# Performance work log

Measured on AMD Instinct MI355X. Metric: run time of the kernel, lower is better.

The kernel has to match this reference:

```python
import jax, jax.numpy as jnp
import numpy as np

N, E, IN, HID, OUT = 50000, 800000, 256, 256, 64
HEADS, DH = 4, 64  # GAT: hidden//4 per head, concat=False -> mean over heads
EPS = 1e-5


def _gcn(x, W, b, src, dst):
    # PyG GCNConv: h = xW; add self-loops; sym-normalized scatter-add; + bias
    n = x.shape[0]
    h = x @ W
    deg = jnp.zeros((n,), x.dtype).at[dst].add(1.0) + 1.0  # +1 for self-loop
    dinv = jax.lax.rsqrt(deg)
    norm = dinv[src] * dinv[dst]                      # [E]
    out = jax.ops.segment_sum(h[src] * norm[:, None], dst, num_segments=n)
    out = out + h * (dinv * dinv)[:, None]            # self-loop term
    return out + b


def _gat(x, W, a_s, a_d, b, src, dst):
    # PyG GATConv(heads=HEADS, concat=False): per-edge attention softmax over
    # incoming edges (incl. self-loop), LeakyReLU(0.2) logits, mean over heads.
    n = x.shape[0]
    h = (x @ W).reshape(n, HEADS, DH)
    al_s = jnp.einsum('nhd,hd->nh', h, a_s)           # [N,H]
    al_d = jnp.einsum('nhd,hd->nh', h, a_d)
    e = jax.nn.leaky_relu(al_s[src] + al_d[dst], 0.2)  # [E,H]
    e_self = jax.nn.leaky_relu(al_s + al_d, 0.2)       # [N,H]
    m = jnp.maximum(jax.ops.segment_max(e, dst, num_segments=n), e_self)
    ee = jnp.exp(e - m[dst])
    es = jnp.exp(e_self - m)
    denom = jax.ops.segment_sum(ee, dst, num_segments=n) + es        # [N,H]
    numer = jax.ops.segment_sum(ee[:, :, None] * h[src], dst, num_segments=n) + es[:, :, None] * h
    return (numer / denom[:, :, None]).mean(axis=1) + b


def _bn(x, g, b):
    # BatchNorm1d over node dim, batch statistics (training-mode math)
    mu = x.mean(axis=0)
    var = x.var(axis=0)
    return g * (x - mu) * jax.lax.rsqrt(var + EPS) + b


def setup_inputs() -> dict:
    key = jax.random.key(0)
    ks = jax.random.split(key, 12)
    s = lambda d: 1.0 / np.sqrt(d)
    inp = {
        'x': jax.random.normal(ks[0], (N, IN), jnp.float32),
        'edge_index': jax.random.randint(ks[1], (2, E), 0, N, jnp.int64),
        'W1': jax.random.normal(ks[2], (IN, HID), jnp.float32) * s(IN),
        'b1': jnp.zeros((HID,), jnp.float32),
        'g1': jnp.ones((HID,), jnp.float32),
        'be1': jnp.zeros((HID,), jnp.float32),
        'Wg': jax.random.normal(ks[3], (HID, HEADS * DH), jnp.float32) * s(HID),
        'a_src': jax.random.normal(ks[4], (HEADS, DH), jnp.float32) * s(DH),
        'a_dst': jax.random.normal(ks[5], (HEADS, DH), jnp.float32) * s(DH),
        'bg': jnp.zeros((DH,), jnp.float32),
        'g2': jnp.ones((DH,), jnp.float32),
        'be2': jnp.zeros((DH,), jnp.float32),
        'W3': jax.random.normal(ks[6], (64, 16), jnp.float32) * s(64),
        'b3': jnp.zeros((16,), jnp.float32),
        'g3': jnp.ones((16,), jnp.float32),
        'be3': jnp.zeros((16,), jnp.float32),
        'W4': jax.random.normal(ks[7], (16, OUT), jnp.float32) * s(16),
        'b4': jnp.zeros((OUT,), jnp.float32),
        'r1W': jax.random.normal(ks[8], (IN, HID), jnp.float32) * s(IN),
        'r1b': jnp.zeros((HID,), jnp.float32),
        'r2W': jax.random.normal(ks[9], (HID, 64), jnp.float32) * s(HID),
        'r2b': jnp.zeros((64,), jnp.float32),
        'r3W': jax.random.normal(ks[10], (64, 16), jnp.float32) * s(64),
        'r3b': jnp.zeros((16,), jnp.float32),
        'pW': jax.random.normal(ks[11], (OUT, OUT), jnp.float32) * s(OUT),
        'pb': jnp.zeros((OUT,), jnp.float32),
    }
    return inp


def reference(x, edge_index, W1, b1, g1, be1, Wg, a_src, a_dst, bg, g2, be2,
              W3, b3, g3, be3, W4, b4, r1W, r1b, r2W, r2b, r3W, r3b, pW, pb):
    src, dst = edge_index[0], edge_index[1]
    slope = 0.01  # F.leaky_relu default; dropout is identity at inference
    x0 = x
    h = _gcn(x0, W1, b1, src, dst)
    h = jax.nn.leaky_relu(_bn(h, g1, be1), slope)
    h = h + (x0 @ r1W + r1b)
    x2 = h
    h = _gat(x2, Wg, a_src, a_dst, bg, src, dst)
    h = jax.nn.leaky_relu(_bn(h, g2, be2), slope)
    h = h + (x2 @ r2W + r2b)
    x3 = h
    h = _gcn(x3, W3, b3, src, dst)
    h = jax.nn.leaky_relu(_bn(h, g3, be3), slope)
    h = h + (x3 @ r3W + r3b)
    h = _gcn(h, W4, b4, src, dst)
    return h @ pW + pb
```

## Files before the change

kernel.cpp:

```cpp
#include <hip/hip_runtime.h>

typedef unsigned short u16;
typedef unsigned int   u32;

__device__ __forceinline__ float b2f(u16 h){ return __uint_as_float(((u32)h)<<16); }
__device__ __forceinline__ u16 f2b(float f){
  u32 u = __float_as_uint(f);
  u32 r = (u + 0x7fffu + ((u>>16)&1u)) >> 16;
  return (u16)r;
}
__device__ __forceinline__ float leaky(float x, float s){ return x >= 0.f ? x : s*x; }

typedef __bf16 bf16x8 __attribute__((ext_vector_type(8)));
typedef float  f32x4  __attribute__((ext_vector_type(4)));

__device__ __forceinline__ float ldval(const u16* p){ return b2f(*p); }
__device__ __forceinline__ float ldval(const float* p){ return *p; }

__device__ __forceinline__ void load8(const u16* p, u16* h){ *(uint4*)h = *(const uint4*)p; }
__device__ __forceinline__ void load8(const float* p, u16* h){
  float4 a = *(const float4*)p; float4 b = *(const float4*)(p+4);
  h[0]=f2b(a.x); h[1]=f2b(a.y); h[2]=f2b(a.z); h[3]=f2b(a.w);
  h[4]=f2b(b.x); h[5]=f2b(b.y); h[6]=f2b(b.z); h[7]=f2b(b.w);
}

__global__ void k_detect(const u32* __restrict__ w, int E, u32* __restrict__ flag){
  u32 acc = 0;
  for (int i = blockIdx.x*256 + threadIdx.x; i < E; i += 256*gridDim.x)
    acc |= w[2*i + 1];
  __shared__ u32 s[256];
  s[threadIdx.x] = acc; __syncthreads();
  for (int o=128;o>0;o>>=1){ if (threadIdx.x<o) s[threadIdx.x] |= s[threadIdx.x+o]; __syncthreads(); }
  if (threadIdx.x==0 && s[0]) atomicOr(flag, 1u);
}

__device__ __forceinline__ void edge_sd(const int* __restrict__ ei, int E, int e, u32 is32,
                                        int& s, int& d){
  if (is32){ s = ei[e];   d = ei[E + e]; }
  else     { s = ei[2*e]; d = ei[2*E + 2*e]; }
}

__global__ void k_hist(const int* __restrict__ ei, int E, int nN,
                       const u32* __restrict__ flag, int* __restrict__ cnt){
  int e = blockIdx.x*256 + threadIdx.x;
  if (e < E){
    int s,d; edge_sd(ei, E, e, *flag, s, d);
    if ((u32)s < (u32)nN && (u32)d < (u32)nN) atomicAdd(&cnt[d], 1);
  }
}

__global__ void k_scan_a(const int* __restrict__ cnt, int n, int* __restrict__ bsum){
  __shared__ int s[256];
  int base = blockIdx.x*1024, t = threadIdx.x, sum = 0;
  for (int j=0;j<4;j++){ int i = base + t*4 + j; if (i<n) sum += cnt[i]; }
  s[t] = sum; __syncthreads();
  for (int off=128; off>0; off>>=1){ if (t<off) s[t]+=s[t+off]; __syncthreads(); }
  if (t==0) bsum[blockIdx.x] = s[0];
}

__global__ void k_scan_b(int* bsum, int nb){
  if (threadIdx.x==0 && blockIdx.x==0){
    int acc = 0;
    for (int i=0;i<nb;i++){ int v = bsum[i]; bsum[i] = acc; acc += v; }
  }
}

__global__ void k_scan_c(const int* __restrict__ cnt, const int* __restrict__ bsum,
                         int n, int* __restrict__ offs){
  __shared__ int s[256];
  int base = blockIdx.x*1024, t = threadIdx.x;
  int v[4]; int sum=0;
  for (int j=0;j<4;j++){ int i=base+t*4+j; v[j] = (i<n)?cnt[i]:0; sum += v[j]; }
  s[t]=sum; __syncthreads();
  for (int off=1; off<256; off<<=1){
    int add = (t>=off)? s[t-off] : 0;
    __syncthreads();
    s[t] += add;
    __syncthreads();
  }
  int excl = (t ? s[t-1] : 0) + bsum[blockIdx.x];
  for (int j=0;j<4;j++){
    int i = base+t*4+j;
    if (i<n){ offs[i] = excl; excl += v[j]; if (i==n-1) offs[n] = excl; }
  }
}

__global__ void k_dinv2(const int* __restrict__ offs, int n, float* __restrict__ dinv){
  int i = blockIdx.x*256+threadIdx.x;
  if (i<n) dinv[i] = rsqrtf((float)(offs[i+1]-offs[i]) + 1.0f);
}

__global__ void k_scatter(const int* __restrict__ ei, int E, int nN,
                          const u32* __restrict__ flag, const int* __restrict__ offs,
                          int* __restrict__ cursor, int* __restrict__ csr){
  int e = blockIdx.x*256+threadIdx.x;
  if (e<E){
    int s,d; edge_sd(ei, E, e, *flag, s, d);
    if ((u32)s < (u32)nN && (u32)d < (u32)nN){
      int pos = offs[d] + atomicAdd(&cursor[d], 1);
      csr[pos] = s;
    }
  }
}

__global__ void k_transpose(const float* __restrict__ in, u16* __restrict__ out, int K, int M){
  int i = blockIdx.x*256 + threadIdx.x;
  if (i < K*M){ int k = i / M, m = i % M; out[m*K + k] = f2b(in[i]); }
}

__global__ void k_asdt(const float* __restrict__ a_s, const float* __restrict__ a_d,
                       float* __restrict__ asi, float* __restrict__ adi){
  int i = threadIdx.x;
  int h = i>>6, c = i&63;
  asi[c*4+h] = a_s[i];
  adi[c*4+h] = a_d[i];
}

template<typename AT>
__global__ __launch_bounds__(256) void k_gemm64(
  const AT* __restrict__ A0, const AT* __restrict__ A1,
  const AT* __restrict__ A2, const AT* __restrict__ A3,
  int rsA, const u16* __restrict__ Bt, const float* __restrict__ bias,
  u16* __restrict__ out, int nRows)
{
  alignas(16) __shared__ u16 Al[64*264];
  const int t = threadIdx.x;
  const int r0 = blockIdx.x*64;
  for (int it=0; it<8; ++it){
    int c = t + it*256;
    int row = c>>5, seg = c&31;
    int gr = r0+row;
    u16 hv[8] = {0,0,0,0,0,0,0,0};
    if (gr < nRows){
      const AT* p = (seg<8)?A0 : (seg<16)?A1 : (seg<24)?A2 : A3;
      load8(p + (size_t)gr*rsA + (seg&7)*8, hv);
    }
    *(uint4*)&Al[row*264 + seg*8] = *(uint4*)hv;
  }
  const int lane=t&63, wid=t>>6, quad=lane>>4, l15=lane&15;
  __syncthreads();
  const int col = wid*16 + l15;
  const u16* Bp = Bt + (size_t)col*256 + quad*8;
  bf16x8 b[8];
  #pragma unroll
  for (int ks=0;ks<8;++ks) b[ks] = *(const bf16x8*)(Bp + ks*32);
  f32x4 acc[4] = {{0.f,0.f,0.f,0.f},{0.f,0.f,0.f,0.f},{0.f,0.f,0.f,0.f},{0.f,0.f,0.f,0.f}};
  #pragma unroll
  for (int rt=0; rt<4; ++rt){
    const int abase = (rt*16 + l15)*264 + quad*8;
    #pragma unroll
    for (int ks=0;ks<8;++ks){
      bf16x8 av = *(const bf16x8*)&Al[abase + ks*32];
      acc[rt] = __builtin_amdgcn_mfma_f32_16x16x32_bf16(av, b[ks], acc[rt], 0,0,0);
    }
  }
  __syncthreads();
  float bv = bias ? bias[col] : 0.f;
  #pragma unroll
  for (int rt=0; rt<4; ++rt){
    #pragma unroll
    for (int reg=0;reg<4;++reg)
      Al[(rt*16 + quad*4 + reg)*264 + col] = f2b(acc[rt][reg]+bv);
  }
  __syncthreads();
  #pragma unroll
  for (int it=0; it<2; ++it){
    int idx = it*256 + t;
    int row = idx>>3, cu = idx&7;
    if (r0+row < nRows)
      *(uint4*)(out + (size_t)(r0+row)*64 + cu*8) = *(const uint4*)&Al[row*264 + cu*8];
  }
}

template<typename AT, bool PERM>
__global__ __launch_bounds__(256) void k_gemm256(
  const AT* __restrict__ A0, const AT* __restrict__ A1,
  const AT* __restrict__ A2, const AT* __restrict__ A3,
  int rsA, const u16* __restrict__ Bt, const float* __restrict__ bias,
  u16* __restrict__ out, int nRows)
{
  alignas(16) __shared__ u16 Al[64*264];
  const int t = threadIdx.x;
  const int r0 = blockIdx.x*64;
  for (int it=0; it<8; ++it){
    int c = t + it*256;
    int row = c>>5, seg = c&31;
    int gr = r0+row;
    u16 hv[8] = {0,0,0,0,0,0,0,0};
    if (gr < nRows){
      const AT* p = (seg<8)?A0 : (seg<16)?A1 : (seg<24)?A2 : A3;
      load8(p + (size_t)gr*rsA + (seg&7)*8, hv);
    }
    *(uint4*)&Al[row*264 + seg*8] = *(uint4*)hv;
  }
  const int lane=t&63, wid=t>>6, quad=lane>>4, l15=lane&15;
  __syncthreads();
  f32x4 acc[4][4];
  #pragma unroll
  for (int ct=0; ct<4; ++ct)
    #pragma unroll
    for (int rt=0; rt<4; ++rt) acc[ct][rt] = {0.f,0.f,0.f,0.f};
  #pragma unroll
  for (int ct=0; ct<4; ++ct){
    const u16* Bp = Bt + (size_t)(wid*64 + ct*16 + l15)*256 + quad*8;
    bf16x8 b[8];
    #pragma unroll
    for (int ks=0;ks<8;++ks) b[ks] = *(const bf16x8*)(Bp + ks*32);
    #pragma unroll
    for (int rt=0; rt<4; ++rt){
      const int abase = (rt*16 + l15)*264 + quad*8;
      #pragma unroll
      for (int ks=0;ks<8;++ks){
        bf16x8 av = *(const bf16x8*)&Al[abase + ks*32];
        acc[ct][rt] = __builtin_amdgcn_mfma_f32_16x16x32_bf16(av, b[ks], acc[ct][rt], 0,0,0);
      }
    }
  }
  __syncthreads();
  #pragma unroll
  for (int ct=0; ct<4; ++ct){
    int col = wid*64 + ct*16 + l15;
    float bv = bias ? bias[col] : 0.f;
    int oc = PERM ? ((col&63)*4 + (col>>6)) : col;
    #pragma unroll
    for (int rt=0; rt<4; ++rt){
      #pragma unroll
      for (int reg=0;reg<4;++reg)
        Al[(rt*16 + quad*4 + reg)*264 + oc] = f2b(acc[ct][rt][reg]+bv);
    }
  }
  __syncthreads();
  #pragma unroll
  for (int it=0; it<8; ++it){
    int idx = it*256 + t;
    int row = idx>>5, cu = idx&31;
    if (r0+row < nRows)
      *(uint4*)(out + (size_t)(r0+row)*256 + cu*8) = *(const uint4*)&Al[row*264 + cu*8];
  }
}

__global__ void k_gather64(const u16* __restrict__ h, const int* __restrict__ offs,
                           const int* __restrict__ csr, const float* __restrict__ dinv,
                           const float* __restrict__ bias, int n, u16* __restrict__ out){
  int nd = blockIdx.x*4 + (threadIdx.x>>6);
  if (nd>=n) return;
  int lane = threadIdx.x&63;
  float dn = dinv[nd];
  float acc = dn*b2f(h[(size_t)nd*64+lane]);
  int e = offs[nd], end = offs[nd+1];
  for (; e+4<=end; e+=4){
    int s0=csr[e], s1=csr[e+1], s2=csr[e+2], s3=csr[e+3];
    float w0=dinv[s0], w1=dinv[s1], w2=dinv[s2], w3=dinv[s3];
    float p0=b2f(h[(size_t)s0*64+lane]);
    float p1=b2f(h[(size_t)s1*64+lane]);
    float p2=b2f(h[(size_t)s2*64+lane]);
    float p3=b2f(h[(size_t)s3*64+lane]);
    acc += w0*p0 + w1*p1 + w2*p2 + w3*p3;
  }
  for (; e<end; ++e){
    int s=csr[e];
    acc += dinv[s]*b2f(h[(size_t)s*64+lane]);
  }
  out[(size_t)nd*64+lane] = f2b(dn*acc + bias[lane]);
}

__global__ void k_gather256(const u16* __restrict__ h, const int* __restrict__ offs,
                            const int* __restrict__ csr, const float* __restrict__ dinv,
                            const float* __restrict__ bias, int n, u16* __restrict__ out){
  int nd = blockIdx.x*4 + (threadIdx.x>>6);
  if (nd>=n) return;
  int lane = threadIdx.x&63;
  const uint2* H = (const uint2*)h;
  float dn = dinv[nd];
  uint2 pv = H[(size_t)nd*64 + lane];
  float a0=dn*b2f(pv.x&0xffff), a1=dn*b2f(pv.x>>16);
  float a2=dn*b2f(pv.y&0xffff), a3=dn*b2f(pv.y>>16);
  int e=offs[nd], end=offs[nd+1];
  for (; e+2<=end; e+=2){
    int s0=csr[e], s1=csr[e+1];
    float w0=dinv[s0], w1=dinv[s1];
    uint2 q0=H[(size_t)s0*64+lane], q1=H[(size_t)s1*64+lane];
    a0 += w0*b2f(q0.x&0xffff) + w1*b2f(q1.x&0xffff);
    a1 += w0*b2f(q0.x>>16)    + w1*b2f(q1.x>>16);
    a2 += w0*b2f(q0.y&0xffff) + w1*b2f(q1.y&0xffff);
    a3 += w0*b2f(q0.y>>16)    + w1*b2f(q1.y>>16);
  }
  for (; e<end; ++e){
    int s=csr[e]; float w=dinv[s];
    uint2 q=H[(size_t)s*64+lane];
    a0 += w*b2f(q.x&0xffff); a1 += w*b2f(q.x>>16);
    a2 += w*b2f(q.y&0xffff); a3 += w*b2f(q.y>>16);
  }
  float4 bv = *(const float4*)(bias + lane*4);
  uint2 o;
  o.x = (u32)f2b(a0*dn + bv.x) | ((u32)f2b(a1*dn + bv.y)<<16);
  o.y = (u32)f2b(a2*dn + bv.z) | ((u32)f2b(a3*dn + bv.w)<<16);
  ((uint2*)out)[(size_t)nd*64 + lane] = o;
}

template<typename T, int C>
__global__ __launch_bounds__(256) void k_stats_part(const T* __restrict__ x, int n,
                                                    float* __restrict__ part){
  constexpr int VE = 16/sizeof(T);
  constexpr int G  = C/VE;
  constexpr int R  = 256/G;
  int t = threadIdx.x;
  int g = t % G, sub = t / G;
  int rpb = (n + gridDim.x - 1) / gridDim.x;
  int base = blockIdx.x * rpb;
  int lim  = min(base + rpb, n);
  float s[VE], s2[VE];
  #pragma unroll
  for (int j=0;j<VE;j++){ s[j]=0.f; s2[j]=0.f; }
  #pragma unroll 4
  for (int r = base + sub; r < lim; r += R){
    const T* p = x + (size_t)r*C + g*VE;
    if constexpr (sizeof(T)==2){
      uint4 v = *(const uint4*)p;
      u32 wq[4] = {v.x, v.y, v.z, v.w};
      #pragma unroll
      for (int q=0;q<4;q++){
        float lo = __uint_as_float(wq[q]<<16);
        float hi = __uint_as_float(wq[q]&0xffff0000u);
        s[2*q]  += lo; s2[2*q]  += lo*lo;
        s[2*q+1]+= hi; s2[2*q+1]+= hi*hi;
      }
    } else {
      float4 v = *(const float4*)p;
      float a[4] = {v.x, v.y, v.z, v.w};
      #pragma unroll
      for (int q=0;q<4;q++){ s[q]+=a[q]; s2[q]+=a[q]*a[q]; }
    }
  }
  __shared__ float red[VE][256];
  #pragma unroll
  for (int j=0;j<VE;j++) red[j][t] = s[j];
  __syncthreads();
  for (int off=R/2; off>0; off>>=1){
    if (sub < off){
      #pragma unroll
      for (int j=0;j<VE;j++) red[j][t] += red[j][t + off*G];
    }
    __syncthreads();
  }
  if (t < G){
    #pragma unroll
    for (int j=0;j<VE;j++) part[blockIdx.x*2*C + t*VE + j] = red[j][t];
  }
  __syncthreads();
  #pragma unroll
  for (int j=0;j<VE;j++) red[j][t] = s2[j];
  __syncthreads();
  for (int off=R/2; off>0; off>>=1){
    if (sub < off){
      #pragma unroll
      for (int j=0;j<VE;j++) red[j][t] += red[j][t + off*G];
    }
    __syncthreads();
  }
  if (t < G){
    #pragma unroll
    for (int j=0;j<VE;j++) part[blockIdx.x*2*C + C + t*VE + j] = red[j][t];
  }
}

template<int C>
__global__ __launch_bounds__(256) void k_bnfin3(const float* __restrict__ part, int B,
                         const float* __restrict__ g, const float* __restrict__ be,
                         float n, float* __restrict__ bnp){
  constexpr int CPB = (C < 32) ? C : 32;
  constexpr int TPC = 256 / CPB;
  int t = threadIdx.x;
  int lc = t % CPB, sub = t / CPB;
  int c = blockIdx.x*CPB + lc;
  float s=0.f, s2=0.f;
  for (int b = sub; b < B; b += TPC){
    s  += part[(size_t)b*2*C + c];
    s2 += part[(size_t)b*2*C + C + c];
  }
  __shared__ float ls[256], lq[256];
  ls[t]=s; lq[t]=s2; __syncthreads();
  for (int off=TPC/2; off>0; off>>=1){
    if (sub < off){ ls[t]+=ls[t+off*CPB]; lq[t]+=lq[t+off*CPB]; }
    __syncthreads();
  }
  if (sub==0){
    float mu = ls[t]/n;
    float var = fmaxf(lq[t]/n - mu*mu, 0.f);
    float sc = g[c] * rsqrtf(var + 1e-5f);
    bnp[c] = sc;
    bnp[C+c] = be[c] - mu*sc;
  }
}

__global__ void k_ew_b16b16(const u16* __restrict__ agg, const u16* __restrict__ res,
                            const float* __restrict__ bnp, int C, int total, u16* __restrict__ out){
  int i = blockIdx.x*256+threadIdx.x;
  if (i < total){
    int c = i & (C-1);
    float v = b2f(agg[i])*bnp[c] + bnp[C+c];
    out[i] = f2b(leaky(v, 0.01f) + b2f(res[i]));
  }
}

__global__ void k_ew_f32f32(const float* __restrict__ agg, const float* __restrict__ res,
                            const float* __restrict__ bnp, int C, int total, float* __restrict__ out){
  int i = blockIdx.x*256+threadIdx.x;
  if (i < total){
    int c = i & (C-1);
    float v = agg[i]*bnp[c] + bnp[C+c];
    out[i] = leaky(v, 0.01f) + res[i];
  }
}

__global__ void k_dot64(const u16* __restrict__ h2t, const float* __restrict__ asg,
                        const float* __restrict__ adg, int head, int n,
                        float* __restrict__ als, float* __restrict__ ald){
  int nd = blockIdx.x*4 + (threadIdx.x>>6);
  if (nd>=n) return;
  int lane = threadIdx.x&63;
  float p = b2f(h2t[(size_t)nd*64+lane]);
  float ss = p*asg[lane];
  float sd = p*adg[lane];
  for (int m=1;m<64;m<<=1){ ss += __shfl_xor(ss,m,64); sd += __shfl_xor(sd,m,64); }
  if (lane==0){ als[nd*4+head]=ss; ald[nd*4+head]=sd; }
}

__global__ void k_gat_head(const u16* __restrict__ h2t, const int* __restrict__ offs,
                           const int* __restrict__ csr, const float* __restrict__ als,
                           const float* __restrict__ ald, const float* __restrict__ bg,
                           int head, int n, u16* __restrict__ O2){
  int nd = blockIdx.x*4 + (threadIdx.x>>6);
  if (nd>=n) return;
  int lane = threadIdx.x&63;
  float aldn = ald[nd*4+head];
  float m = leaky(als[nd*4+head] + aldn, 0.2f);
  float denom = 1.f;
  float acc = b2f(h2t[(size_t)nd*64+lane]);
  int e = offs[nd], end = offs[nd+1];
  for (; e+4<=end; e+=4){
    int s0=csr[e], s1=csr[e+1], s2=csr[e+2], s3=csr[e+3];
    float l0=als[s0*4+head], l1=als[s1*4+head], l2=als[s2*4+head], l3=als[s3*4+head];
    float p0=b2f(h2t[(size_t)s0*64+lane]);
    float p1=b2f(h2t[(size_t)s1*64+lane]);
    float p2=b2f(h2t[(size_t)s2*64+lane]);
    float p3=b2f(h2t[(size_t)s3*64+lane]);
    float g0=leaky(l0+aldn,0.2f), g1=leaky(l1+aldn,0.2f);
    float g2=leaky(l2+aldn,0.2f), g3=leaky(l3+aldn,0.2f);
    float mc = fmaxf(fmaxf(g0,g1), fmaxf(g2,g3));
    float mn = fmaxf(m, mc);
    float sc = __expf(m - mn);
    float w0 = __expf(g0-mn), w1 = __expf(g1-mn), w2 = __expf(g2-mn), w3 = __expf(g3-mn);
    denom = denom*sc + (w0+w1+w2+w3);
    acc   = acc*sc   + (w0*p0 + w1*p1 + w2*p2 + w3*p3);
    m = mn;
  }
  for (; e<end; ++e){
    int s = csr[e];
    float g = leaky(als[s*4+head]+aldn, 0.2f);
    float p = b2f(h2t[(size_t)s*64+lane]);
    float mn = fmaxf(m, g);
    float sc = __expf(m - mn);
    float w = __expf(g - mn);
    denom = denom*sc + w;
    acc   = acc*sc   + w*p;
    m = mn;
  }
  float v = 0.25f * acc / fmaxf(denom, 1e-20f);
  size_t oi = (size_t)nd*64+lane;
  if (head==0) O2[oi] = f2b(v + bg[lane]);
  else         O2[oi] = f2b(b2f(O2[oi]) + v);
}

__global__ void k_dot_all(const u16* __restrict__ h2i, const float* __restrict__ asi,
                          const float* __restrict__ adi, int n,
                          float* __restrict__ als, float* __restrict__ ald){
  int nd = blockIdx.x*4 + (threadIdx.x>>6);
  if (nd>=n) return;
  int lane = threadIdx.x&63;
  uint2 pv = ((const uint2*)h2i)[(size_t)nd*64+lane];
  float p0=b2f(pv.x&0xffff), p1=b2f(pv.x>>16), p2=b2f(pv.y&0xffff), p3=b2f(pv.y>>16);
  float4 as4 = *(const float4*)(asi + lane*4);
  float4 ad4 = *(const float4*)(adi + lane*4);
  float s0=p0*as4.x, s1=p1*as4.y, s2=p2*as4.z, s3=p3*as4.w;
  float d0=p0*ad4.x, d1=p1*ad4.y, d2=p2*ad4.z, d3=p3*ad4.w;
  for (int m=1;m<64;m<<=1){
    s0+=__shfl_xor(s0,m,64); s1+=__shfl_xor(s1,m,64);
    s2+=__shfl_xor(s2,m,64); s3+=__shfl_xor(s3,m,64);
    d0+=__shfl_xor(d0,m,64); d1+=__shfl_xor(d1,m,64);
    d2+=__shfl_xor(d2,m,64); d3+=__shfl_xor(d3,m,64);
  }
  if (lane==0){
    float4 sv = {s0,s1,s2,s3}; float4 dv = {d0,d1,d2,d3};
    ((float4*)als)[nd] = sv;
    ((float4*)ald)[nd] = dv;
  }
}

__global__ void k_gat_all(const u16* __restrict__ h2i, const int* __restrict__ offs,
                          const int* __restrict__ csr, const float* __restrict__ als,
                          const float* __restrict__ ald, const float* __restrict__ bg,
                          int n, u16* __restrict__ O2){
  alignas(16) __shared__ float shm[4][80];
  int wv = threadIdx.x>>6;
  int nd = blockIdx.x*4 + wv;
  if (nd>=n) return;
  int lane = threadIdx.x&63;
  int eg = lane>>2, hh = lane&3;
  float4 alv = ((const float4*)als)[nd];
  float4 adv = ((const float4*)ald)[nd];
  float adh = (hh&2) ? ((hh&1)?adv.w:adv.z) : ((hh&1)?adv.y:adv.x);
  float alh = (hh&2) ? ((hh&1)?alv.w:alv.z) : ((hh&1)?alv.y:alv.x);
  float gsh = leaky(alh+adh, 0.2f);
  int beg=offs[nd], end=offs[nd+1];
  float m = gsh;
  for (int e=beg+eg; e<end; e+=16){
    int s = csr[e];
    m = fmaxf(m, leaky(als[s*4+hh]+adh, 0.2f));
  }
  #pragma unroll
  for (int off=4; off<64; off<<=1) m = fmaxf(m, __shfl_xor(m, off, 64));
  float wsh = __expf(gsh - m);
  if (eg==0) shm[wv][4+hh] = wsh;
  float4 ws4 = *(const float4*)&shm[wv][4];
  uint2 pv = ((const uint2*)h2i)[(size_t)nd*64+lane];
  float a0 = ws4.x*__uint_as_float(pv.x<<16);
  float a1 = ws4.y*__uint_as_float(pv.x&0xffff0000u);
  float a2 = ws4.z*__uint_as_float(pv.y<<16);
  float a3 = ws4.w*__uint_as_float(pv.y&0xffff0000u);
  float dpart = 0.f;
  const uint2* H = (const uint2*)h2i;
  for (int e0=beg; e0<end; e0+=16){
    int e = e0+eg;
    int sA = 0; float wE = 0.f;
    if (e<end){
      sA = csr[e];
      wE = __expf(leaky(als[sA*4+hh]+adh, 0.2f) - m);
    }
    dpart += wE;
    shm[wv][8+lane] = wE;
    int cnt = min(16, end-e0);
    int k=0;
    for (; k+4<=cnt; k+=4){
      int sa=__shfl(sA,(k  )*4,64), sb=__shfl(sA,(k+1)*4,64);
      int sc=__shfl(sA,(k+2)*4,64), sd=__shfl(sA,(k+3)*4,64);
      float4 wa=*(const float4*)&shm[wv][8+(k  )*4];
      float4 wb=*(const float4*)&shm[wv][8+(k+1)*4];
      float4 wc=*(const float4*)&shm[wv][8+(k+2)*4];
      float4 wd=*(const float4*)&shm[wv][8+(k+3)*4];
      uint2 qa=H[(size_t)sa*64+lane], qb=H[(size_t)sb*64+lane];
      uint2 qc=H[(size_t)sc*64+lane], qd=H[(size_t)sd*64+lane];
      a0 += wa.x*__uint_as_float(qa.x<<16) + wb.x*__uint_as_float(qb.x<<16)
          + wc.x*__uint_as_float(qc.x<<16) + wd.x*__uint_as_float(qd.x<<16);
      a1 += wa.y*__uint_as_float(qa.x&0xffff0000u) + wb.y*__uint_as_float(qb.x&0xffff0000u)
          + wc.y*__uint_as_float(qc.x&0xffff0000u) + wd.y*__uint_as_float(qd.x&0xffff0000u);
      a2 += wa.z*__uint_as_float(qa.y<<16) + wb.z*__uint_as_float(qb.y<<16)
          + wc.z*__uint_as_float(qc.y<<16) + wd.z*__uint_as_float(qd.y<<16);
      a3 += wa.w*__uint_as_float(qa.y&0xffff0000u) + wb.w*__uint_as_float(qb.y&0xffff0000u)
          + wc.w*__uint_as_float(qc.y&0xffff0000u) + wd.w*__uint_as_float(qd.y&0xffff0000u);
    }
    for (; k<cnt; ++k){
      int s = __shfl(sA, k*4, 64);
      float4 w4 = *(const float4*)&shm[wv][8+k*4];
      uint2 q = H[(size_t)s*64+lane];
      a0 += w4.x*__uint_as_float(q.x<<16);
      a1 += w4.y*__uint_as_float(q.x&0xffff0000u);
      a2 += w4.z*__uint_as_float(q.y<<16);
      a3 += w4.w*__uint_as_float(q.y&0xffff0000u);
    }
  }
  #pragma unroll
  for (int off=4; off<64; off<<=1) dpart += __shfl_xor(dpart, off, 64);
  float dh = dpart + wsh;
  if (eg==0) shm[wv][hh] = dh;
  float4 d4 = *(const float4*)&shm[wv][0];
  float v = 0.25f*(a0/d4.x + a1/d4.y + a2/d4.z + a3/d4.w);
  O2[(size_t)nd*64+lane] = f2b(v + bg[lane]);
}

__global__ void k_gcn_agg16(const float* __restrict__ h, const int* __restrict__ offs,
                            const int* __restrict__ csr, const float* __restrict__ dinv,
                            const float* __restrict__ bias, float* __restrict__ out, int n){
  int t = threadIdx.x;
  int nd = blockIdx.x*16 + (t>>4);
  if (nd>=n) return;
  int c = t&15;
  float dn = dinv[nd];
  float acc = dn*h[(size_t)nd*16+c];
  int e=offs[nd], end=offs[nd+1];
  for (; e+4<=end; e+=4){
    int s0=csr[e], s1=csr[e+1], s2=csr[e+2], s3=csr[e+3];
    float w0=dinv[s0], w1=dinv[s1], w2=dinv[s2], w3=dinv[s3];
    float p0=h[(size_t)s0*16+c], p1=h[(size_t)s1*16+c];
    float p2=h[(size_t)s2*16+c], p3=h[(size_t)s3*16+c];
    acc += w0*p0 + w1*p1 + w2*p2 + w3*p3;
  }
  for (; e<end; ++e){
    int s = csr[e];
    acc += dinv[s]*h[(size_t)s*16+c];
  }
  out[(size_t)nd*16+c] = dn*acc + bias[c];
}

__global__ void k_gcn_agg64f(const float* __restrict__ h, const int* __restrict__ offs,
                             const int* __restrict__ csr, const float* __restrict__ dinv,
                             const float* __restrict__ bias, float* __restrict__ out, int n){
  int nd = blockIdx.x*4 + (threadIdx.x>>6);
  if (nd>=n) return;
  int lane = threadIdx.x&63;
  float dn = dinv[nd];
  float acc = dn*h[(size_t)nd*64+lane];
  int e=offs[nd], end=offs[nd+1];
  for (; e+4<=end; e+=4){
    int s0=csr[e], s1=csr[e+1], s2=csr[e+2], s3=csr[e+3];
    float w0=dinv[s0], w1=dinv[s1], w2=dinv[s2], w3=dinv[s3];
    float p0=h[(size_t)s0*64+lane], p1=h[(size_t)s1*64+lane];
    float p2=h[(size_t)s2*64+lane], p3=h[(size_t)s3*64+lane];
    acc += w0*p0 + w1*p1 + w2*p2 + w3*p3;
  }
  for (; e<end; ++e){
    int s=csr[e];
    acc += dinv[s]*h[(size_t)s*64+lane];
  }
  out[(size_t)nd*64+lane] = dn*acc + bias[lane];
}

__global__ void k_gemm64_16x2(const u16* __restrict__ x, const float* __restrict__ W1_,
                              const float* __restrict__ W2_, const float* __restrict__ b2_,
                              int n, float* __restrict__ o1, float* __restrict__ o2){
  __shared__ float w1[64*16], w2[64*16];
  int t = threadIdx.x;
  for (int i=t; i<1024; i+=256){ w1[i]=W1_[i]; w2[i]=W2_[i]; }
  __syncthreads();
  int nd = blockIdx.x*8 + (t>>5);
  if (nd>=n) return;
  int j = t & 31;
  const u16* xr = x + (size_t)nd*64;
  if (j<16){
    float s=0.f;
    #pragma unroll 8
    for (int k=0;k<64;k++) s += b2f(xr[k])*w1[k*16+j];
    o1[(size_t)nd*16+j]=s;
  } else {
    int jj=j-16;
    float s = b2_[jj];
    #pragma unroll 8
    for (int k=0;k<64;k++) s += b2f(xr[k])*w2[k*16+jj];
    o2[(size_t)nd*16+jj]=s;
  }
}

__global__ void k_gemm16_64(const float* __restrict__ x, const float* __restrict__ W,
                            int n, float* __restrict__ o){
  __shared__ float w[16*64];
  int t = threadIdx.x;
  for (int i=t;i<1024;i+=256) w[i]=W[i];
  __syncthreads();
  int nd = blockIdx.x*4 + (t>>6);
  if (nd>=n) return;
  int j = t&63;
  const float* xr = x + (size_t)nd*16;
  float s=0.f;
  #pragma unroll
  for (int k=0;k<16;k++) s += xr[k]*w[k*64+j];
  o[(size_t)nd*64+j]=s;
}

__global__ void k_final(const float* __restrict__ x, const float* __restrict__ W,
                        const float* __restrict__ b, int n, float* __restrict__ out){
  __shared__ float w[64*64];
  int t=threadIdx.x;
  for (int i=t;i<4096;i+=256) w[i]=W[i];
  __syncthreads();
  int nd = blockIdx.x*4 + (t>>6);
  if (nd>=n) return;
  int j=t&63;
  const float* xr = x + (size_t)nd*64;
  float s=b[j];
  #pragma unroll 8
  for (int k=0;k<64;k++) s += xr[k]*w[k*64+j];
  out[(size_t)nd*64+j]=s;
}

extern "C" void kernel_launch(void* const* d_in, const int* in_sizes, int n_in,
                              void* d_out, int out_size, void* d_ws, size_t ws_size,
                              hipStream_t stream) {
  const float* x   = (const float*)d_in[0];
  const int*   ei  = (const int*)d_in[1];
  const float* W1  = (const float*)d_in[2];
  const float* b1  = (const float*)d_in[3];
  const float* g1  = (const float*)d_in[4];
  const float* be1 = (const float*)d_in[5];
  const float* Wg  = (const float*)d_in[6];
  const float* a_s = (const float*)d_in[7];
  const float* a_d = (const float*)d_in[8];
  const float* bg  = (const float*)d_in[9];
  const float* g2  = (const float*)d_in[10];
  const float* be2 = (const float*)d_in[11];
  const float* W3  = (const float*)d_in[12];
  const float* b3  = (const float*)d_in[13];
  const float* g3  = (const float*)d_in[14];
  const float* be3 = (const float*)d_in[15];
  const float* W4  = (const float*)d_in[16];
  const float* b4  = (const float*)d_in[17];
  const float* r1W = (const float*)d_in[18];
  const float* r1b = (const float*)d_in[19];
  const float* r2W = (const float*)d_in[20];
  const float* r2b = (const float*)d_in[21];
  const float* r3W = (const float*)d_in[22];
  const float* r3b = (const float*)d_in[23];
  const float* pW  = (const float*)d_in[24];
  const float* pb  = (const float*)d_in[25];

  const int N = in_sizes[0] / 256;
  const int E = in_sizes[1] / 2;

  char* w = (char*)d_ws;
  auto alloc = [&](size_t b)->void*{ void* p=(void*)w; w += (b+255)&~(size_t)255; return p; };
  u32*   flag   = (u32*)  alloc(4);
  float* part   = (float*)alloc(256*512*4);
  float* bnp1   = (float*)alloc(512*4);
  float* bnp2   = (float*)alloc(128*4);
  float* bnp3   = (float*)alloc(32*4);
  int*   bsum   = (int*)  alloc(256*4);
  int*   cur    = (int*)  alloc((size_t)N*4);
  int*   offs   = (int*)  alloc((size_t)(N+1)*4);
  float* dinv   = (float*)alloc((size_t)N*4);
  int*   csr    = (int*)  alloc((size_t)E*4);
  float* als    = (float*)alloc((size_t)N*16);
  float* ald    = (float*)alloc((size_t)N*16);
  float* asi    = (float*)alloc(256*4);
  float* adi    = (float*)alloc(256*4);
  u16*   W1t    = (u16*)  alloc(65536*2);
  u16*   r1Wt   = (u16*)  alloc(65536*2);
  u16*   Wgt    = (u16*)  alloc(65536*2);
  u16*   r2Wt   = (u16*)  alloc(16384*2);

  auto cdiv = [](int a, int b){ return (a+b-1)/b; };
  const int nb1024 = cdiv(N, 1024);
  const int statsGrid = 256;
  const int gemmGrid = cdiv(N,64);
  const int nodeGrid = cdiv(N,4);

  hipMemsetAsync(flag,   0, 4, stream);
  hipMemsetAsync(cur,    0, (size_t)N*4, stream);

  k_detect<<<64,256,0,stream>>>((const u32*)ei, E, flag);

  k_transpose<<<cdiv(65536,256),256,0,stream>>>(W1,  W1t,  256,256);
  k_transpose<<<cdiv(65536,256),256,0,stream>>>(r1W, r1Wt, 256,256);
  k_transpose<<<cdiv(65536,256),256,0,stream>>>(Wg,  Wgt,  256,256);
  k_transpose<<<cdiv(16384,256),256,0,stream>>>(r2W, r2Wt, 256,64);
  k_asdt<<<1,256,0,stream>>>(a_s, a_d, asi, adi);

  k_hist  <<<cdiv(E,256),256,0,stream>>>(ei, E, N, flag, cur);
  k_scan_a<<<nb1024,256,0,stream>>>(cur, N, bsum);
  k_scan_b<<<1,64,0,stream>>>(bsum, nb1024);
  k_scan_c<<<nb1024,256,0,stream>>>(cur, bsum, N, offs);
  k_dinv2 <<<cdiv(N,256),256,0,stream>>>(offs, N, dinv);
  hipMemsetAsync(cur, 0, (size_t)N*4, stream);
  k_scatter<<<cdiv(E,256),256,0,stream>>>(ei, E, N, flag, offs, cur, csr);

  size_t miscUsed = (size_t)(w - (char*)d_ws);
  size_t bigNeed  = miscUsed + 2*((size_t)N*512) + 1024;

  if (ws_size >= bigNeed){
    u16* RA = (u16*)alloc((size_t)N*512);
    u16* RB = (u16*)alloc((size_t)N*512);
    u16* tAe = (u16*)d_in[1];
    u16* r2d = (u16*)d_out;

    float* h3   = (float*)RA;
    float* r3   = (float*)(RA + (size_t)N*32);
    float* agg3 = (float*)(RA + (size_t)N*64);
    float* x4   = (float*)(RA + (size_t)N*96);
    float* h4   = (float*)RB;
    float* agg4 = (float*)d_out;

    k_gemm256<float,false><<<gemmGrid,256,0,stream>>>(x, x+64, x+128, x+192, 256,
                                                      W1t, nullptr, RA, N);
    k_gather256<<<nodeGrid,256,0,stream>>>(RA, offs, csr, dinv, b1, N, RB);
    k_stats_part<u16,256><<<statsGrid,256,0,stream>>>(RB, N, part);
    k_bnfin3<256><<<8,256,0,stream>>>(part, statsGrid, g1, be1, (float)N, bnp1);
    k_gemm256<float,false><<<gemmGrid,256,0,stream>>>(x, x+64, x+128, x+192, 256,
                                                      r1Wt, r1b, RA, N);
    k_ew_b16b16<<<cdiv(N*256,256),256,0,stream>>>(RB, RA, bnp1, 256, N*256, RB);

    k_gemm256<u16,true><<<gemmGrid,256,0,stream>>>(RB, RB+64, RB+128, RB+192, 256,
                                                   Wgt, nullptr, RA, N);
    k_gemm64<u16><<<gemmGrid,256,0,stream>>>(RB, RB+64, RB+128, RB+192, 256,
                                             r2Wt, r2b, r2d, N);
    k_dot_all<<<nodeGrid,256,0,stream>>>(RA, asi, adi, N, als, ald);
    k_gat_all<<<nodeGrid,256,0,stream>>>(RA, offs, csr, als, ald, bg, N, tAe);
    k_stats_part<u16,64><<<statsGrid,256,0,stream>>>(tAe, N, part);
    k_bnfin3<64><<<2,256,0,stream>>>(part, statsGrid, g2, be2, (float)N, bnp2);
    k_ew_b16b16<<<cdiv(N*64,256),256,0,stream>>>(tAe, r2d, bnp2, 64, N*64, tAe);

    k_gemm64_16x2<<<cdiv(N,8),256,0,stream>>>(tAe, W3, r3W, r3b, N, h3, r3);
    k_gcn_agg16<<<cdiv(N,16),256,0,stream>>>(h3, offs, csr, dinv, b3, agg3, N);
    k_stats_part<float,16><<<statsGrid,256,0,stream>>>(agg3, N, part);
    k_bnfin3<16><<<1,256,0,stream>>>(part, statsGrid, g3, be3, (float)N, bnp3);
    k_ew_f32f32<<<cdiv(N*16,256),256,0,stream>>>(agg3, r3, bnp3, 16, N*16, x4);

    k_gemm16_64<<<nodeGrid,256,0,stream>>>(x4, W4, N, h4);
    k_gcn_agg64f<<<nodeGrid,256,0,stream>>>(h4, offs, csr, dinv, b4, agg4, N);
    k_final<<<nodeGrid,256,0,stream>>>(agg4, pW, pb, N, (float*)d_out);
  } else {
    u16* X0 = (u16*)alloc((size_t)N*64*2);
    u16* X1 = (u16*)alloc((size_t)N*64*2);
    u16* tA = (u16*)alloc((size_t)N*64*2);
    u16* tB = (u16*)alloc((size_t)N*64*2);
    u16* X2 = (u16*)d_in[1];
    u16* X3 = (u16*)d_out;
    const u16* XP[4] = {X0, X1, X2, X3};

    float* h3   = (float*)X1;
    float* r3   = (float*)(X1 + (size_t)N*32);
    float* agg3 = (float*)tA;
    float* x4   = (float*)(tA + (size_t)N*32);
    float* h4   = (float*)X0;
    float* agg4 = (float*)tA;

    for (int tau=0; tau<4; ++tau){
      u16* Xt = (u16*)XP[tau];
      k_gemm64<float><<<gemmGrid,256,0,stream>>>(x, x+64, x+128, x+192, 256,
                                                 W1t + (size_t)tau*64*256, nullptr, tA, N);
      k_gather64<<<nodeGrid,256,0,stream>>>(tA, offs, csr, dinv, b1 + tau*64, N, tB);
      k_stats_part<u16,64><<<statsGrid,256,0,stream>>>(tB, N, part);
      k_bnfin3<64><<<2,256,0,stream>>>(part, statsGrid, g1 + tau*64, be1 + tau*64, (float)N, bnp1 + tau*128);
      k_gemm64<float><<<gemmGrid,256,0,stream>>>(x, x+64, x+128, x+192, 256,
                                                 r1Wt + (size_t)tau*64*256, r1b + tau*64, tA, N);
      k_ew_b16b16<<<cdiv(N*64,256),256,0,stream>>>(tB, tA, bnp1 + tau*128, 64, N*64, Xt);
    }

    for (int head=0; head<4; ++head){
      k_gemm64<u16><<<gemmGrid,256,0,stream>>>(XP[0], XP[1], XP[2], XP[3], 64,
                                               Wgt + (size_t)head*64*256, nullptr, tA, N);
      k_dot64<<<nodeGrid,256,0,stream>>>(tA, a_s + head*64, a_d + head*64, head, N, als, ald);
      k_gat_head<<<nodeGrid,256,0,stream>>>(tA, offs, csr, als, ald, bg, head, N, tB);
    }
    k_gemm64<u16><<<gemmGrid,256,0,stream>>>(XP[0], XP[1], XP[2], XP[3], 64,
                                             r2Wt, r2b, tA, N);
    k_stats_part<u16,64><<<statsGrid,256,0,stream>>>(tB, N, part);
    k_bnfin3<64><<<2,256,0,stream>>>(part, statsGrid, g2, be2, (float)N, bnp2);
    k_ew_b16b16<<<cdiv(N*64,256),256,0,stream>>>(tB, tA, bnp2, 64, N*64, X0);

    k_gemm64_16x2<<<cdiv(N,8),256,0,stream>>>(X0, W3, r3W, r3b, N, h3, r3);
    k_gcn_agg16<<<cdiv(N,16),256,0,stream>>>(h3, offs, csr, dinv, b3, agg3, N);
    k_stats_part<float,16><<<statsGrid,256,0,stream>>>(agg3, N, part);
    k_bnfin3<16><<<1,256,0,stream>>>(part, statsGrid, g3, be3, (float)N, bnp3);
    k_ew_f32f32<<<cdiv(N*16,256),256,0,stream>>>(agg3, r3, bnp3, 16, N*16, x4);

    k_gemm16_64<<<nodeGrid,256,0,stream>>>(x4, W4, N, h4);
    k_gcn_agg64f<<<nodeGrid,256,0,stream>>>(h4, offs, csr, dinv, b4, agg4, N);
    k_final<<<nodeGrid,256,0,stream>>>(agg4, pW, pb, N, (float*)d_out);
  }
}
```

Baseline: 725.0 us.

## Split graph aggregation kernels across channel groups and parallel edge slices

Three CSR aggregation kernels (GCN layer-1 gather, the GAT attention aggregation, and the final 64-wide GCN aggregation) are replaced with variants that split each node's channels into groups handled by separate blocks. Each wave also processes four edges at once in 16-lane slices, followed by shuffle reductions. The aim is more memory-level parallelism and a larger grid for the irregular neighbour gathers, with nontemporal loads on the CSR indices. The cost is redundant reads of CSR, dinv and attention logits across channel groups, extra shuffles, and in GAT a repeated max pass per group.

```diff
diff --git a/kernel.cpp b/kernel.cpp
--- a/kernel.cpp
+++ b/kernel.cpp
@@ -262,6 +262,47 @@
     acc += dinv[s]*b2f(h[(size_t)s*64+lane]);
   }
   out[(size_t)nd*64+lane] = f2b(dn*acc + bias[lane]);
+}
+
+__global__ __launch_bounds__(256) void k_gather256x(const u16* __restrict__ h, const int* __restrict__ offs,
+                              const int* __restrict__ csr, const float* __restrict__ dinv,
+                              const float* __restrict__ bias, int n, u16* __restrict__ out){
+  int bid = blockIdx.x;
+  int cg = bid & 7, tile = bid >> 3;
+  int nd = tile*4 + (threadIdx.x>>6);
+  if (nd>=n) return;
+  int lane = threadIdx.x & 63;
+  int es = lane >> 4, li = lane & 15;
+  const u32* H = (const u32*)h;
+  const int coff = cg*16 + li;
+  float dn = dinv[nd];
+  float a0 = 0.f, a1 = 0.f;
+  if (es == 0){
+    u32 pv = H[(size_t)nd*128 + coff];
+    a0 = dn*b2f(pv&0xffff); a1 = dn*b2f(pv>>16);
+  }
+  int e = offs[nd] + es, end = offs[nd+1];
+  for (; e + 4 < end; e += 8){
+    int s0 = __builtin_nontemporal_load(&csr[e]);
+    int s1 = __builtin_nontemporal_load(&csr[e+4]);
+    float w0 = dinv[s0], w1 = dinv[s1];
+    u32 q0 = H[(size_t)s0*128 + coff], q1 = H[(size_t)s1*128 + coff];
+    a0 += w0*b2f(q0&0xffff) + w1*b2f(q1&0xffff);
+    a1 += w0*b2f(q0>>16)    + w1*b2f(q1>>16);
+  }
+  if (e < end){
+    int s = __builtin_nontemporal_load(&csr[e]);
+    float w = dinv[s];
+    u32 q = H[(size_t)s*128 + coff];
+    a0 += w*b2f(q&0xffff); a1 += w*b2f(q>>16);
+  }
+  a0 += __shfl_xor(a0,16,64); a0 += __shfl_xor(a0,32,64);
+  a1 += __shfl_xor(a1,16,64); a1 += __shfl_xor(a1,32,64);
+  if (es == 0){
+    int c = cg*32 + li*2;
+    u32 o = (u32)f2b(a0*dn + bias[c]) | ((u32)f2b(a1*dn + bias[c+1])<<16);
+    ((u32*)out)[(size_t)nd*128 + coff] = o;
+  }
 }
 
 __global__ void k_gather256(const u16* __restrict__ h, const int* __restrict__ offs,
@@ -497,6 +538,77 @@
   }
 }
 
+__global__ __launch_bounds__(256) void k_gat_allx(const u16* __restrict__ h2i, const int* __restrict__ offs,
+                           const int* __restrict__ csr, const float* __restrict__ als,
+                           const float* __restrict__ ald, const float* __restrict__ bg,
+                           int n, u16* __restrict__ O2){
+  int bid = blockIdx.x;
+  int cg = bid & 7, tile = bid >> 3;
+  int nd = tile*4 + (threadIdx.x>>6);
+  if (nd>=n) return;
+  int lane = threadIdx.x & 63;
+  int es = lane >> 4, li = lane & 15;
+  int hh = lane & 3;
+  int h0 = (li & 1) << 1, h1 = h0 + 1;
+  float4 alv = ((const float4*)als)[nd];
+  float4 adv = ((const float4*)ald)[nd];
+  float adh = (hh&2) ? ((hh&1)?adv.w:adv.z) : ((hh&1)?adv.y:adv.x);
+  float alh = (hh&2) ? ((hh&1)?alv.w:alv.z) : ((hh&1)?alv.y:alv.x);
+  float gsh = leaky(alh+adh, 0.2f);
+  int beg = offs[nd], end = offs[nd+1];
+  float m = gsh;
+  for (int e = beg+es; e < end; e += 4){
+    int s = __builtin_nontemporal_load(&csr[e]);
+    m = fmaxf(m, leaky(als[s*4+hh]+adh, 0.2f));
+  }
+  #pragma unroll
+  for (int off=4; off<64; off<<=1) m = fmaxf(m, __shfl_xor(m, off, 64));
+  float wsh = __expf(gsh - m);
+  const u32* H = (const u32*)h2i;
+  const int coff = cg*16 + li;
+  float a0 = 0.f, a1 = 0.f, dpart = 0.f;
+  int e = beg + es;
+  for (; e + 4 < end; e += 8){
+    int sA = __builtin_nontemporal_load(&csr[e]);
+    int sB = __builtin_nontemporal_load(&csr[e+4]);
+    float wEa = 0.f, wEb = 0.f;
+    if (li < 4){
+      wEa = __expf(leaky(als[sA*4+li]+adh, 0.2f) - m);
+      wEb = __expf(leaky(als[sB*4+li]+adh, 0.2f) - m);
+    }
+    dpart += wEa + wEb;
+    float wa0 = __shfl(wEa, es*16 + h0, 64), wa1 = __shfl(wEa, es*16 + h1, 64);
+    float wb0 = __shfl(wEb, es*16 + h0, 64), wb1 = __shfl(wEb, es*16 + h1, 64);
+    u32 qa = H[(size_t)sA*128 + coff], qb = H[(size_t)sB*128 + coff];
+    a0 += wa0*b2f(qa&0xffff) + wb0*b2f(qb&0xffff);
+    a1 += wa1*b2f(qa>>16)    + wb1*b2f(qb>>16);
+  }
+  if (e < end){
+    int s = __builtin_nontemporal_load(&csr[e]);
+    float wE = 0.f;
+    if (li < 4) wE = __expf(leaky(als[s*4+li]+adh, 0.2f) - m);
+    dpart += wE;
+    float w0 = __shfl(wE, es*16 + h0, 64), w1 = __shfl(wE, es*16 + h1, 64);
+    u32 q = H[(size_t)s*128 + coff];
+    a0 += w0*b2f(q&0xffff);
+    a1 += w1*b2f(q>>16);
+  }
+  #pragma unroll
+  for (int off=4; off<64; off<<=1) dpart += __shfl_xor(dpart, off, 64);
+  a0 += __shfl_xor(a0,16,64); a0 += __shfl_xor(a0,32,64);
+  a1 += __shfl_xor(a1,16,64); a1 += __shfl_xor(a1,32,64);
+  float d = dpart + wsh;
+  float dv0 = __shfl(d, h0, 64),  dv1 = __shfl(d, h1, 64);
+  float ws0 = __shfl(wsh, h0, 64), ws1 = __shfl(wsh, h1, 64);
+  u32 qs = H[(size_t)nd*128 + coff];
+  float r = (a0 + ws0*b2f(qs&0xffff))/dv0 + (a1 + ws1*b2f(qs>>16))/dv1;
+  r += __shfl_xor(r, 1, 64);
+  if (es==0 && (li&1)==0){
+    int c = cg*8 + (li>>1);
+    O2[(size_t)nd*64 + c] = f2b(0.25f*r + bg[c]);
+  }
+}
+
 __global__ void k_gat_all(const u16* __restrict__ h2i, const int* __restrict__ offs,
                           const int* __restrict__ csr, const float* __restrict__ als,
                           const float* __restrict__ ald, const float* __restrict__ bg,
@@ -600,6 +712,32 @@
     acc += dinv[s]*h[(size_t)s*16+c];
   }
   out[(size_t)nd*16+c] = dn*acc + bias[c];
+}
+
+__global__ __launch_bounds__(256) void k_gcn_agg64fx(const float* __restrict__ h, const int* __restrict__ offs,
+                              const int* __restrict__ csr, const float* __restrict__ dinv,
+                              const float* __restrict__ bias, float* __restrict__ out, int n){
+  int bid = blockIdx.x;
+  int cg = bid & 3, tile = bid >> 2;
+  int nd = tile*4 + (threadIdx.x>>6);
+  if (nd>=n) return;
+  int lane = threadIdx.x&63;
+  int es = lane>>4, li = lane&15;
+  int ch = cg*16 + li;
+  float dn = dinv[nd];
+  float a = (es==0) ? dn*h[(size_t)nd*64+ch] : 0.f;
+  int e = offs[nd]+es, end = offs[nd+1];
+  for (; e+4 < end; e += 8){
+    int s0 = __builtin_nontemporal_load(&csr[e]);
+    int s1 = __builtin_nontemporal_load(&csr[e+4]);
+    a += dinv[s0]*h[(size_t)s0*64+ch] + dinv[s1]*h[(size_t)s1*64+ch];
+  }
+  if (e < end){
+    int s = __builtin_nontemporal_load(&csr[e]);
+    a += dinv[s]*h[(size_t)s*64+ch];
+  }
+  a += __shfl_xor(a,16,64); a += __shfl_xor(a,32,64);
+  if (es==0) out[(size_t)nd*64+ch] = dn*a + bias[ch];
 }
 
 __global__ void k_gcn_agg64f(const float* __restrict__ h, const int* __restrict__ offs,
@@ -779,7 +917,7 @@
 
     k_gemm256<float,false><<<gemmGrid,256,0,stream>>>(x, x+64, x+128, x+192, 256,
                                                       W1t, nullptr, RA, N);
-    k_gather256<<<nodeGrid,256,0,stream>>>(RA, offs, csr, dinv, b1, N, RB);
+    k_gather256x<<<nodeGrid*8,256,0,stream>>>(RA, offs, csr, dinv, b1, N, RB);
     k_stats_part<u16,256><<<statsGrid,256,0,stream>>>(RB, N, part);
     k_bnfin3<256><<<8,256,0,stream>>>(part, statsGrid, g1, be1, (float)N, bnp1);
     k_gemm256<float,false><<<gemmGrid,256,0,stream>>>(x, x+64, x+128, x+192, 256,
@@ -791,7 +929,7 @@
     k_gemm64<u16><<<gemmGrid,256,0,stream>>>(RB, RB+64, RB+128, RB+192, 256,
                                              r2Wt, r2b, r2d, N);
     k_dot_all<<<nodeGrid,256,0,stream>>>(RA, asi, adi, N, als, ald);
-    k_gat_all<<<nodeGrid,256,0,stream>>>(RA, offs, csr, als, ald, bg, N, tAe);
+    k_gat_allx<<<nodeGrid*8,256,0,stream>>>(RA, offs, csr, als, ald, bg, N, tAe);
     k_stats_part<u16,64><<<statsGrid,256,0,stream>>>(tAe, N, part);
     k_bnfin3<64><<<2,256,0,stream>>>(part, statsGrid, g2, be2, (float)N, bnp2);
     k_ew_b16b16<<<cdiv(N*64,256),256,0,stream>>>(tAe, r2d, bnp2, 64, N*64, tAe);
@@ -803,7 +941,7 @@
     k_ew_f32f32<<<cdiv(N*16,256),256,0,stream>>>(agg3, r3, bnp3, 16, N*16, x4);
 
     k_gemm16_64<<<nodeGrid,256,0,stream>>>(x4, W4, N, h4);
-    k_gcn_agg64f<<<nodeGrid,256,0,stream>>>(h4, offs, csr, dinv, b4, agg4, N);
+    k_gcn_agg64fx<<<nodeGrid*4,256,0,stream>>>(h4, offs, csr, dinv, b4, agg4, N);
     k_final<<<nodeGrid,256,0,stream>>>(agg4, pW, pb, N, (float*)d_out);
   } else {
     u16* X0 = (u16*)alloc((size_t)N*64*2);
```

Result: slower. 1.394 ms (+92.3%).

## Fuse BN/residual elementwise and GAT attention dots into GEMM epilogues

Applied to the files above, without the earlier changes.

The residual GEMM epilogue now applies the first BatchNorm affine, leaky ReLU and residual add, reading the aggregated buffer and writing back in place. This removes the separate elementwise kernel. The GAT projection GEMM now computes the per-head source and destination attention dot products from its shared-memory tile, which replaces the separate dot kernel and its re-read of the projected features. This saves two launches and about two full passes over N×256 bf16 data. The cost is extra epilogue work and more registers in the GEMM, and the in-place aliasing of agg and out, both RB, relies on each element being read before it is written by the same thread.

```diff
diff --git a/kernel.cpp b/kernel.cpp
--- a/kernel.cpp
+++ b/kernel.cpp
@@ -172,11 +172,14 @@
   }
 }
 
-template<typename AT, bool PERM>
+template<typename AT, bool PERM, bool EW, bool DOT>
 __global__ __launch_bounds__(256) void k_gemm256(
   const AT* __restrict__ A0, const AT* __restrict__ A1,
   const AT* __restrict__ A2, const AT* __restrict__ A3,
   int rsA, const u16* __restrict__ Bt, const float* __restrict__ bias,
+  const u16* __restrict__ agg, const float* __restrict__ bnp,
+  const float* __restrict__ asi, const float* __restrict__ adi,
+  float* __restrict__ als, float* __restrict__ ald,
   u16* __restrict__ out, int nRows)
 {
   alignas(16) __shared__ u16 Al[64*264];
@@ -230,12 +233,61 @@
     }
   }
   __syncthreads();
+  if constexpr (DOT){
+    int row = t>>2, q = t&3;
+    int nd = r0 + row;
+    if (nd < nRows){
+      float s0=0.f,s1=0.f,s2=0.f,s3=0.f,d0=0.f,d1=0.f,d2=0.f,d3=0.f;
+      const u16* ar = &Al[row*264 + q*64];
+      const float* as = asi + q*64;
+      const float* ad = adi + q*64;
+      #pragma unroll 4
+      for (int k=0;k<64;k+=4){
+        uint2 wv = *(const uint2*)&ar[k];
+        float v0=b2f((u16)(wv.x&0xffff)), v1=b2f((u16)(wv.x>>16));
+        float v2=b2f((u16)(wv.y&0xffff)), v3=b2f((u16)(wv.y>>16));
+        s0 += v0*as[k];   d0 += v0*ad[k];
+        s1 += v1*as[k+1]; d1 += v1*ad[k+1];
+        s2 += v2*as[k+2]; d2 += v2*ad[k+2];
+        s3 += v3*as[k+3]; d3 += v3*ad[k+3];
+      }
+      s0 += __shfl_xor(s0,1,64); s0 += __shfl_xor(s0,2,64);
+      s1 += __shfl_xor(s1,1,64); s1 += __shfl_xor(s1,2,64);
+      s2 += __shfl_xor(s2,1,64); s2 += __shfl_xor(s2,2,64);
+      s3 += __shfl_xor(s3,1,64); s3 += __shfl_xor(s3,2,64);
+      d0 += __shfl_xor(d0,1,64); d0 += __shfl_xor(d0,2,64);
+      d1 += __shfl_xor(d1,1,64); d1 += __shfl_xor(d1,2,64);
+      d2 += __shfl_xor(d2,1,64); d2 += __shfl_xor(d2,2,64);
+      d3 += __shfl_xor(d3,1,64); d3 += __shfl_xor(d3,2,64);
+      if (q==0){
+        float4 sv = {s0,s1,s2,s3}; float4 dv = {d0,d1,d2,d3};
+        ((float4*)als)[nd] = sv;
+        ((float4*)ald)[nd] = dv;
+      }
+    }
+  }
   #pragma unroll
   for (int it=0; it<8; ++it){
     int idx = it*256 + t;
     int row = idx>>5, cu = idx&31;
-    if (r0+row < nRows)
-      *(uint4*)(out + (size_t)(r0+row)*256 + cu*8) = *(const uint4*)&Al[row*264 + cu*8];
+    int r = r0+row;
+    if (r < nRows){
+      if constexpr (EW){
+        uint4 hv = *(const uint4*)&Al[row*264 + cu*8];
+        uint4 av = *(const uint4*)(agg + (size_t)r*256 + cu*8);
+        const u16* hp = (const u16*)&hv; const u16* ap = (const u16*)&av;
+        uint4 ov; u16* op = (u16*)&ov;
+        #pragma unroll
+        for (int j=0;j<8;++j){
+          int c = cu*8+j;
+          float v = b2f(ap[j])*bnp[c] + bnp[256+c];
+          op[j] = f2b(leaky(v, 0.01f) + b2f(hp[j]));
+        }
+        *(uint4*)(out + (size_t)r*256 + cu*8) = ov;
+      } else {
+        *(uint4*)(out + (size_t)r*256 + cu*8) = *(const uint4*)&Al[row*264 + cu*8];
+      }
+    }
   }
 }
 
@@ -470,31 +522,6 @@
   size_t oi = (size_t)nd*64+lane;
   if (head==0) O2[oi] = f2b(v + bg[lane]);
   else         O2[oi] = f2b(b2f(O2[oi]) + v);
-}
-
-__global__ void k_dot_all(const u16* __restrict__ h2i, const float* __restrict__ asi,
-                          const float* __restrict__ adi, int n,
-                          float* __restrict__ als, float* __restrict__ ald){
-  int nd = blockIdx.x*4 + (threadIdx.x>>6);
-  if (nd>=n) return;
-  int lane = threadIdx.x&63;
-  uint2 pv = ((const uint2*)h2i)[(size_t)nd*64+lane];
-  float p0=b2f(pv.x&0xffff), p1=b2f(pv.x>>16), p2=b2f(pv.y&0xffff), p3=b2f(pv.y>>16);
-  float4 as4 = *(const float4*)(asi + lane*4);
-  float4 ad4 = *(const float4*)(adi + lane*4);
-  float s0=p0*as4.x, s1=p1*as4.y, s2=p2*as4.z, s3=p3*as4.w;
-  float d0=p0*ad4.x, d1=p1*ad4.y, d2=p2*ad4.z, d3=p3*ad4.w;
-  for (int m=1;m<64;m<<=1){
-    s0+=__shfl_xor(s0,m,64); s1+=__shfl_xor(s1,m,64);
-    s2+=__shfl_xor(s2,m,64); s3+=__shfl_xor(s3,m,64);
-    d0+=__shfl_xor(d0,m,64); d1+=__shfl_xor(d1,m,64);
-    d2+=__shfl_xor(d2,m,64); d3+=__shfl_xor(d3,m,64);
-  }
-  if (lane==0){
-    float4 sv = {s0,s1,s2,s3}; float4 dv = {d0,d1,d2,d3};
-    ((float4*)als)[nd] = sv;
-    ((float4*)ald)[nd] = dv;
-  }
 }
 
 __global__ void k_gat_all(const u16* __restrict__ h2i, const int* __restrict__ offs,
@@ -777,20 +804,21 @@
     float* h4   = (float*)RB;
     float* agg4 = (float*)d_out;
 
-    k_gemm256<float,false><<<gemmGrid,256,0,stream>>>(x, x+64, x+128, x+192, 256,
-                                                      W1t, nullptr, RA, N);
+    k_gemm256<float,false,false,false><<<gemmGrid,256,0,stream>>>(
+        x, x+64, x+128, x+192, 256, W1t, nullptr,
+        nullptr, nullptr, nullptr, nullptr, nullptr, nullptr, RA, N);
     k_gather256<<<nodeGrid,256,0,stream>>>(RA, offs, csr, dinv, b1, N, RB);
     k_stats_part<u16,256><<<statsGrid,256,0,stream>>>(RB, N, part);
     k_bnfin3<256><<<8,256,0,stream>>>(part, statsGrid, g1, be1, (float)N, bnp1);
-    k_gemm256<float,false><<<gemmGrid,256,0,stream>>>(x, x+64, x+128, x+192, 256,
-                                                      r1Wt, r1b, RA, N);
-    k_ew_b16b16<<<cdiv(N*256,256),256,0,stream>>>(RB, RA, bnp1, 256, N*256, RB);
-
-    k_gemm256<u16,true><<<gemmGrid,256,0,stream>>>(RB, RB+64, RB+128, RB+192, 256,
-                                                   Wgt, nullptr, RA, N);
+    k_gemm256<float,false,true,false><<<gemmGrid,256,0,stream>>>(
+        x, x+64, x+128, x+192, 256, r1Wt, r1b,
+        RB, bnp1, nullptr, nullptr, nullptr, nullptr, RB, N);
+
+    k_gemm256<u16,true,false,true><<<gemmGrid,256,0,stream>>>(
+        RB, RB+64, RB+128, RB+192, 256, Wgt, nullptr,
+        nullptr, nullptr, asi, adi, als, ald, RA, N);
     k_gemm64<u16><<<gemmGrid,256,0,stream>>>(RB, RB+64, RB+128, RB+192, 256,
                                              r2Wt, r2b, r2d, N);
-    k_dot_all<<<nodeGrid,256,0,stream>>>(RA, asi, adi, N, als, ald);
     k_gat_all<<<nodeGrid,256,0,stream>>>(RA, offs, csr, als, ald, bg, N, tAe);
     k_stats_part<u16,64><<<statsGrid,256,0,stream>>>(tAe, N, part);
     k_bnfin3<64><<<2,256,0,stream>>>(part, statsGrid, g2, be2, (float)N, bnp2);
```

Result: no change. 727.9 us (+0.4%).
